# Optimization experiments

Measured on AMD Instinct MI355X. Metric: run time of the kernel, lower is better.

## Reference

```python
import jax, jax.numpy as jnp
import numpy as np

B = 16384          # batch
IN = 256           # input_dim
HID = [1024, 1024, 512]
K = 8              # num_mixtures
D = 16             # latent_dim
NT = D * (D + 1) // 2  # 136 packed tril components per mixture

_rows, _cols = np.tril_indices(D)          # row-major lower-tri order, same as nested loops
_rows = jnp.asarray(_rows); _cols = jnp.asarray(_cols)
_diag_mask = _rows == _cols                # [NT] bool


def setup_inputs() -> dict:
    key = jax.random.key(0)
    ks = jax.random.split(key, 12)

    def lin(k, fi, fo):
        kw, kb = jax.random.split(k)
        s = 1.0 / np.sqrt(fi)
        W = (jax.random.uniform(kw, (fi, fo), minval=-s, maxval=s)).astype(jnp.float32)
        b = (jax.random.uniform(kb, (fo,), minval=-s, maxval=s)).astype(jnp.float32)
        return W, b

    W0, b0 = lin(ks[0], IN, HID[0])
    W1, b1 = lin(ks[1], HID[0], HID[1])
    W2, b2 = lin(ks[2], HID[1], HID[2])
    Wpi, bpi = lin(ks[3], HID[2], K)
    Wmu, bmu = lin(ks[4], HID[2], K * D)
    Wt, bt = lin(ks[5], HID[2], K * NT)
    x = jax.random.normal(ks[6], (B, IN), dtype=jnp.float32)
    return dict(x=x, W0=W0, b0=b0, W1=W1, b1=b1, W2=W2, b2=b2,
                Wpi=Wpi, bpi=bpi, Wmu=Wmu, bmu=bmu, Wt=Wt, bt=bt)


def reference(x, W0, b0, W1, b1, W2, b2, Wpi, bpi, Wmu, bmu, Wt, bt):
    # MLP trunk: Linear + ReLU chain
    h = jax.nn.relu(x @ W0 + b0)
    h = jax.nn.relu(h @ W1 + b1)
    h = jax.nn.relu(h @ W2 + b2)
    # Heads
    pi_k = jax.nn.softmax(h @ Wpi + bpi, axis=1)                 # [B, K]
    mu_k = (h @ Wmu + bmu).reshape(-1, K, D)                     # [B, K, D]
    tc = (h @ Wt + bt).reshape(-1, K, NT)                        # [B, K, NT]
    # Fused cholesky-tril assembly: exp on diagonal entries, copy off-diagonal,
    # scattered into lower triangle in row-major (i, j<=i) order.
    vals = jnp.where(_diag_mask, jnp.exp(tc), tc)                # [B, K, NT]
    tril = jnp.zeros((tc.shape[0], K, D, D), dtype=tc.dtype)
    tril = tril.at[:, :, _rows, _cols].set(vals)                 # [B, K, D, D]
    return pi_k, mu_k, tril
```

## Files before the change

### kernel.cpp

```cpp
#include <hip/hip_runtime.h>
#include <hip/hip_bf16.h>
#include <cstdint>
#include <cstddef>

typedef __attribute__((ext_vector_type(8))) _Float16 half8;
typedef __attribute__((ext_vector_type(4))) float f32x4;
typedef __attribute__((ext_vector_type(8))) unsigned short ushort8v;
typedef __attribute__((ext_vector_type(4))) unsigned short ushort4v;

__device__ __forceinline__ unsigned short f2h_bits(float x) {
  _Float16 h = (_Float16)x;
  union { _Float16 h; unsigned short u; } cv; cv.h = h; return cv.u;
}

__device__ __forceinline__ void barrier_raw() {
  asm volatile("" ::: "memory");
  __builtin_amdgcn_s_barrier();
  asm volatile("" ::: "memory");
}
template<int N> __device__ __forceinline__ void vmw() {
  static_assert(N == 0 || N == 3 || N == 4, "unsupported vmcnt");
  if constexpr (N == 0) asm volatile("s_waitcnt vmcnt(0)" ::: "memory");
  if constexpr (N == 3) asm volatile("s_waitcnt vmcnt(3)" ::: "memory");
  if constexpr (N == 4) asm volatile("s_waitcnt vmcnt(4)" ::: "memory");
}
__device__ __forceinline__ void lgkm0() {
  asm volatile("s_waitcnt lgkmcnt(0)" ::: "memory");
}


__global__ __launch_bounds__(256) void k_f32_to_f16(const float* __restrict__ src,
                                                    unsigned short* __restrict__ dst, int n4) {
  int i = blockIdx.x * 256 + threadIdx.x;
  if (i >= n4) return;
  float4 v = ((const float4*)src)[i];
  ushort4v o;
  o[0] = f2h_bits(v.x); o[1] = f2h_bits(v.y); o[2] = f2h_bits(v.z); o[3] = f2h_bits(v.w);
  ((ushort4v*)dst)[i] = o;
}

__global__ __launch_bounds__(256) void k_transpose_f16(const float* __restrict__ W,
                                                       unsigned short* __restrict__ Wt,
                                                       int Kd, int N) {
  int tid = blockIdx.x * 256 + threadIdx.x;
  int total = (Kd >> 3) * N;
  if (tid >= total) return;
  int kc = tid / N;
  int n  = tid - kc * N;
  int k0 = kc << 3;
  ushort8v o;
#pragma unroll
  for (int j = 0; j < 8; ++j) o[j] = f2h_bits(W[(size_t)(k0 + j) * N + n]);
  *(ushort8v*)(&Wt[(size_t)n * Kd + k0]) = o;
}

__global__ __launch_bounds__(256) void k_build_head(
    const float* __restrict__ Wmu, const float* __restrict__ Wt,
    const float* __restrict__ Wpi,
    const float* __restrict__ bmu, const float* __restrict__ bt,
    const float* __restrict__ bpi,
    unsigned short* __restrict__ whd, float* __restrict__ bhd)
{
  int tid = blockIdx.x * 256 + threadIdx.x;
  if (tid >= 2304 * 64) return;
  int r  = tid >> 6;
  int d0 = (tid & 63) << 3;

  const float* src = nullptr; int stride = 0;
  if (r < 128) { src = Wmu + r; stride = 128; }
  else if (r < 2176) {
    int rU = r - 128, k = rU >> 8, i = (rU >> 4) & 15, j = rU & 15;
    if (j <= i) { src = Wt + k * 136 + ((i * (i + 1)) >> 1) + j; stride = 1088; }
  } else if (r < 2184) { src = Wpi + (r - 2176); stride = 8; }

  ushort8v o;
#pragma unroll
  for (int jj = 0; jj < 8; ++jj)
    o[jj] = src ? f2h_bits(src[(size_t)(d0 + jj) * stride]) : (unsigned short)0;
  *(ushort8v*)(&whd[(size_t)r * 512 + d0]) = o;

  if (d0 == 0) {
    float b = 0.f;
    if (r < 128) b = bmu[r];
    else if (r < 2176) {
      int rU = r - 128, k = rU >> 8, i = (rU >> 4) & 15, j = rU & 15;
      if (j <= i) b = bt[k * 136 + ((i * (i + 1)) >> 1) + j];
    } else if (r < 2184) b = bpi[r - 2176];
    bhd[r] = b;
  }
}


__device__ __forceinline__ void epi_relu_h(const f32x4& a, const float* bias, int col0,
                                           unsigned short* Hout, size_t row, int N) {
  float4 b4 = *(const float4*)&bias[col0];
  ushort4v o;
  float v0 = a[0] + b4.x; o[0] = f2h_bits(v0 > 0.f ? v0 : 0.f);
  float v1 = a[1] + b4.y; o[1] = f2h_bits(v1 > 0.f ? v1 : 0.f);
  float v2 = a[2] + b4.z; o[2] = f2h_bits(v2 > 0.f ? v2 : 0.f);
  float v3 = a[3] + b4.w; o[3] = f2h_bits(v3 > 0.f ? v3 : 0.f);
  *(ushort4v*)&Hout[row * N + col0] = o;
}

__device__ __forceinline__ void epi_head(const f32x4& a, const float* bias, int col0,
                                         size_t row, float* out_pi, float* out_mu,
                                         float* out_tril) {
  if (col0 >= 2184) return;
  float4 b4 = *(const float4*)&bias[col0];
  float v[4] = { a[0] + b4.x, a[1] + b4.y, a[2] + b4.z, a[3] + b4.w };
  if (col0 < 128) {
    *(float4*)&out_mu[row * 128 + col0] = make_float4(v[0], v[1], v[2], v[3]);
  } else if (col0 < 2176) {
    const int cc0 = col0 - 128;
    const int i   = (cc0 >> 4) & 15;
    const int j0  = cc0 & 15;
#pragma unroll
    for (int r = 0; r < 4; ++r) if (j0 + r == i) v[r] = expf(v[r]);
    *(float4*)&out_tril[row * 2048 + cc0] = make_float4(v[0], v[1], v[2], v[3]);
  } else {
    float m4 = fmaxf(fmaxf(v[0], v[1]), fmaxf(v[2], v[3]));
    float mx = fmaxf(m4, __shfl_xor(m4, 16));
    float e[4], s4 = 0.f;
#pragma unroll
    for (int r = 0; r < 4; ++r) { e[r] = expf(v[r] - mx); s4 += e[r]; }
    float sm = s4 + __shfl_xor(s4, 16);
    *(float4*)&out_pi[row * 8 + (col0 - 2176)] =
        make_float4(e[0] / sm, e[1] / sm, e[2] / sm, e[3] / sm);
  }
}


template<int EPI>
__global__ __launch_bounds__(256) void k_gemm3b(
    const unsigned short* __restrict__ A,
    const unsigned short* __restrict__ Bt,
    int Kd, int N, int nNb,
    const float* __restrict__ bias,
    unsigned short* __restrict__ Hout,
    float* __restrict__ out_pi,
    float* __restrict__ out_mu,
    float* __restrict__ out_tril)
{
  __shared__ unsigned short Ald[3][128 * 32];
  __shared__ unsigned short Bld[3][128 * 32];

  const int tid  = threadIdx.x;
  const int lane = tid & 63;
  const int wv   = tid >> 6;
  const int wr   = wv >> 1;
  const int wc   = wv & 1;
  const int l15  = lane & 15;
  const int lk   = lane >> 4;

  const int cpx = gridDim.x >> 3;
  const int bid = blockIdx.x;
  const int swz = (bid & 7) * cpx + (bid >> 3);
  const int bm  = (swz / nNb) << 7;
  const int bn  = (swz % nNb) << 7;

  f32x4 acc[4][4] = {};

  const unsigned short* aBase = A  + (size_t)bm * Kd;
  const unsigned short* bBase = Bt + (size_t)bn * Kd;

  const int xo = ((lk ^ ((l15 >> 1) & 3)) << 3);

  auto stage = [&](int bb, int kt) {
    const int k0 = kt << 5;
#pragma unroll
    for (int i = 0; i < 2; ++i) {
      const int cbase = (wv << 6) + (i << 8);
      const int c_    = cbase + lane;
      const int row   = c_ >> 2;
      const int sc    = (((c_ & 3) ^ ((c_ >> 3) & 3)) << 3);
      __builtin_amdgcn_global_load_lds(
          (const __attribute__((address_space(1))) void*)(aBase + (size_t)row * Kd + k0 + sc),
          (__attribute__((address_space(3))) void*)(&Ald[bb][cbase << 3]),
          16, 0, 0);
      __builtin_amdgcn_global_load_lds(
          (const __attribute__((address_space(1))) void*)(bBase + (size_t)row * Kd + k0 + sc),
          (__attribute__((address_space(3))) void*)(&Bld[bb][cbase << 3]),
          16, 0, 0);
    }
  };

  const int nk = Kd >> 5;
  stage(0, 0);
  stage(1, 1);
  vmw<4>();
  barrier_raw();

  int i0 = 0, i1 = 1, i2 = 2;
  for (int kt = 0; kt < nk; ++kt) {
    if (kt + 2 < nk) stage(i2, kt + 2);

    half8 af[4], bfr[4];
#pragma unroll
    for (int m = 0; m < 4; ++m)
      af[m]  = *(const half8*)&Ald[i0][((wr << 6) + (m << 4) + l15) * 32 + xo];
#pragma unroll
    for (int n = 0; n < 4; ++n)
      bfr[n] = *(const half8*)&Bld[i0][((wc << 6) + (n << 4) + l15) * 32 + xo];

    __builtin_amdgcn_s_setprio(1);
#pragma unroll
    for (int m = 0; m < 4; ++m)
#pragma unroll
      for (int n = 0; n < 4; ++n)
        acc[m][n] = __builtin_amdgcn_mfma_f32_16x16x32_f16(bfr[n], af[m], acc[m][n], 0, 0, 0);
    __builtin_amdgcn_s_setprio(0);

    if (kt + 1 < nk) {
      if (kt + 2 < nk) vmw<4>();
      else             vmw<0>();
      barrier_raw();
    }
    const int t = i0; i0 = i1; i1 = i2; i2 = t;
  }

#pragma unroll
  for (int m = 0; m < 4; ++m) {
    const size_t row = bm + (wr << 6) + (m << 4) + l15;
#pragma unroll
    for (int n = 0; n < 4; ++n) {
      const int col0 = bn + (wc << 6) + (n << 4) + (lk << 2);
      if (EPI == 0) epi_relu_h(acc[m][n], bias, col0, Hout, row, N);
      else          epi_head(acc[m][n], bias, col0, row, out_pi, out_mu, out_tril);
    }
  }
}


template<int NH, int M_rep>
__device__ __forceinline__ void mfma_phase(const half8* af, const half8* bf,
                                           f32x4 (*acc)[4]) {
  __builtin_amdgcn_s_setprio(1);
#pragma unroll
  for (int m = 0; m < M_rep; ++m) {
    acc[m][NH * 2 + 0] = __builtin_amdgcn_mfma_f32_16x16x32_f16(bf[0], af[m], acc[m][NH * 2 + 0], 0, 0, 0);
    acc[m][NH * 2 + 1] = __builtin_amdgcn_mfma_f32_16x16x32_f16(bf[1], af[m], acc[m][NH * 2 + 1], 0, 0, 0);
  }
  __builtin_amdgcn_s_setprio(0);
}

template<int BM, int BN>
__global__ __launch_bounds__(512) void k_gemm8p(
    const unsigned short* __restrict__ A,
    const unsigned short* __restrict__ Bt,
    int Kd, int N, int nNb,
    const float* __restrict__ bias,
    unsigned short* __restrict__ Hout)
{
  constexpr int M_rep = BM / 32;
  constexpr int A_LD  = BM / 128;
  constexpr int B_LD  = BN / 128;
  constexpr int WN    = A_LD + B_LD;

  __shared__ unsigned short Ald[2][2][BM * 32];
  __shared__ unsigned short Bld[2][2][BN * 32];

  const int tid  = threadIdx.x;
  const int lane = tid & 63;
  const int wid  = tid >> 6;
  const int wm   = wid >> 2;
  const int wn   = wid & 3;
  const int l15  = lane & 15;
  const int lk   = lane >> 4;

  const int cpx = gridDim.x >> 3;
  const int bid = blockIdx.x;
  const int swz = (bid & 7) * cpx + (bid >> 3);
  const int bm  = (swz / nNb) * BM;
  const int bn  = (swz % nNb) * BN;

  const unsigned short* aBase = A  + (size_t)bm * Kd;
  const unsigned short* bBase = Bt + (size_t)bn * Kd;

  f32x4 acc[M_rep][4] = {};

  const int xo   = ((lk ^ ((l15 >> 1) & 3)) << 3);
  const int rowA = wm * (BM / 2) + l15;
  const int colB = wn * 64 + l15;

  auto stageA = [&](int bb, int h, int k0) {
#pragma unroll
    for (int i = 0; i < A_LD; ++i) {
      const int cbase = (wid << 6) + (i << 9);
      const int c_    = cbase + lane;
      const int row   = c_ >> 2;
      const int sc    = (((c_ & 3) ^ ((c_ >> 3) & 3)) << 3);
      __builtin_amdgcn_global_load_lds(
          (const __attribute__((address_space(1))) void*)(aBase + (size_t)row * Kd + k0 + h * 32 + sc),
          (__attribute__((address_space(3))) void*)(&Ald[bb][h][(size_t)cbase << 3]),
          16, 0, 0);
    }
  };
  auto stageB = [&](int bb, int h, int k0) {
#pragma unroll
    for (int i = 0; i < B_LD; ++i) {
      const int cbase = (wid << 6) + (i << 9);
      const int c_    = cbase + lane;
      const int row   = c_ >> 2;
      const int sc    = (((c_ & 3) ^ ((c_ >> 3) & 3)) << 3);
      __builtin_amdgcn_global_load_lds(
          (const __attribute__((address_space(1))) void*)(bBase + (size_t)row * Kd + k0 + h * 32 + sc),
          (__attribute__((address_space(3))) void*)(&Bld[bb][h][(size_t)cbase << 3]),
          16, 0, 0);
    }
  };

#define RD_A(kk)                                                                 \
  {                                                                              \
    _Pragma("unroll")                                                            \
    for (int m = 0; m < M_rep; ++m)                                              \
      af[m] = *(const half8*)&Ald[cur][kk][(size_t)(rowA + m * 16) * 32 + xo];   \
  }
#define RD_B(kk, nh)                                                             \
  {                                                                              \
    _Pragma("unroll")                                                            \
    for (int n2 = 0; n2 < 2; ++n2)                                               \
      bf[n2] = *(const half8*)&Bld[cur][kk][(size_t)(colB + ((nh) * 2 + n2) * 16) * 32 + xo]; \
  }

  const int nk = Kd >> 6;
  stageA(0, 0, 0); stageB(0, 0, 0); stageA(0, 1, 0); stageB(0, 1, 0);
  vmw<WN>();
  barrier_raw();

  int cur = 0;
  for (int kt = 0; kt < nk; ++kt) {
    const bool pre = (kt + 1 < nk);
    const int  k0n = (kt + 1) << 6;
    half8 af[M_rep], bf[2];

    RD_A(0); RD_B(0, 0);
    if (pre) stageA(cur ^ 1, 0, k0n);
    barrier_raw(); lgkm0();
    mfma_phase<0, M_rep>(af, bf, acc);
    barrier_raw();

    RD_B(0, 1);
    if (pre) stageB(cur ^ 1, 0, k0n);
    barrier_raw(); lgkm0();
    mfma_phase<1, M_rep>(af, bf, acc);
    if (pre) vmw<WN>(); else vmw<0>();
    barrier_raw();

    RD_A(1); RD_B(1, 0);
    if (pre) stageA(cur ^ 1, 1, k0n);
    barrier_raw(); lgkm0();
    mfma_phase<0, M_rep>(af, bf, acc);
    barrier_raw();

    RD_B(1, 1);
    if (pre) stageB(cur ^ 1, 1, k0n);
    barrier_raw(); lgkm0();
    mfma_phase<1, M_rep>(af, bf, acc);
    if (pre) vmw<WN>();
    barrier_raw();

    cur ^= 1;
  }
#undef RD_A
#undef RD_B

#pragma unroll
  for (int m = 0; m < M_rep; ++m) {
    const size_t row = bm + wm * (BM / 2) + (m << 4) + l15;
#pragma unroll
    for (int n = 0; n < 4; ++n) {
      const int col0 = bn + wn * 64 + (n << 4) + (lk << 2);
      epi_relu_h(acc[m][n], bias, col0, Hout, row, N);
    }
  }
}


extern "C" void kernel_launch(void* const* d_in, const int* in_sizes, int n_in,
                              void* d_out, int out_size, void* d_ws, size_t ws_size,
                              hipStream_t stream)
{
  const float* x   = (const float*)d_in[0];
  const float* W0  = (const float*)d_in[1];
  const float* b0  = (const float*)d_in[2];
  const float* W1  = (const float*)d_in[3];
  const float* b1  = (const float*)d_in[4];
  const float* W2  = (const float*)d_in[5];
  const float* b2  = (const float*)d_in[6];
  const float* Wpi = (const float*)d_in[7];
  const float* bpi = (const float*)d_in[8];
  const float* Wmu = (const float*)d_in[9];
  const float* bmu = (const float*)d_in[10];
  const float* Wt  = (const float*)d_in[11];
  const float* bt  = (const float*)d_in[12];

  char* ws = (char*)d_ws;
  unsigned short* xh  = (unsigned short*)(ws);
  unsigned short* h0  = (unsigned short*)(ws + 8388608);
  unsigned short* h1  = (unsigned short*)(ws + 41943040);
  unsigned short* h2  = (unsigned short*)(ws + 8388608);
  unsigned short* w0b = (unsigned short*)(ws + 75497472);
  unsigned short* w1b = (unsigned short*)(ws + 76021760);
  unsigned short* w2b = (unsigned short*)(ws + 78118912);
  unsigned short* whd = (unsigned short*)(ws + 79167488);
  float*          bhd = (float*)         (ws + 81526784);

  float* out_pi   = (float*)d_out;
  float* out_mu   = (float*)d_out + 131072;
  float* out_tril = (float*)d_out + 2228224;

  k_f32_to_f16<<<4096, 256, 0, stream>>>(x, xh, 1048576);
  k_transpose_f16<<<128, 256, 0, stream>>>(W0, w0b, 256, 1024);
  k_transpose_f16<<<512, 256, 0, stream>>>(W1, w1b, 1024, 1024);
  k_transpose_f16<<<256, 256, 0, stream>>>(W2, w2b, 1024, 512);
  k_build_head<<<576, 256, 0, stream>>>(Wmu, Wt, Wpi, bmu, bt, bpi, whd, bhd);

  k_gemm3b<0><<<1024, 256, 0, stream>>>(xh, w0b, 256, 1024, 8, b0, h0,
                                        nullptr, nullptr, nullptr);
  k_gemm8p<256, 256><<<256, 512, 0, stream>>>(h0, w1b, 1024, 1024, 4, b1, h1);
  k_gemm8p<128, 256><<<256, 512, 0, stream>>>(h1, w2b, 1024, 512, 2, b2, h2);
  k_gemm3b<1><<<2304, 256, 0, stream>>>(h2, whd, 512, 2304, 18, bhd, nullptr,
                                        out_pi, out_mu, out_tril);
}
```

Before: 185.9 us.

## Replace LDS-tiled head GEMM with register-direct MFMA kernel on pre-swizzled weights

Head weights are now pre-packed into the exact per-lane MFMA fragment order, and head columns are padded to 2240 instead of 2304. A new head kernel loads A and B fragments straight from global memory into registers with double buffering, skipping LDS staging and barriers. Blocks are swizzled across 35 column strips so neighbouring blocks share A rows in cache. The aim is to cut LDS traffic, synchronisation and padded work in the output-bound head GEMM. The cost is heavier global and L2 load traffic with no LDS reuse across waves.

```diff
diff --git a/kernel.cpp b/kernel.cpp
--- a/kernel.cpp
+++ b/kernel.cpp
@@ -59,12 +59,13 @@
     const float* __restrict__ Wpi,
     const float* __restrict__ bmu, const float* __restrict__ bt,
     const float* __restrict__ bpi,
-    unsigned short* __restrict__ whd, float* __restrict__ bhd)
+    unsigned short* __restrict__ bsh, float* __restrict__ bhd)
 {
   int tid = blockIdx.x * 256 + threadIdx.x;
-  if (tid >= 2304 * 64) return;
+  if (tid >= 2240 * 64) return;
   int r  = tid >> 6;
-  int d0 = (tid & 63) << 3;
+  int o  = tid & 63;
+  int d0 = o << 3;
 
   const float* src = nullptr; int stride = 0;
   if (r < 128) { src = Wmu + r; stride = 128; }
@@ -73,13 +74,21 @@
     if (j <= i) { src = Wt + k * 136 + ((i * (i + 1)) >> 1) + j; stride = 1088; }
   } else if (r < 2184) { src = Wpi + (r - 2176); stride = 8; }
 
-  ushort8v o;
+  ushort8v ov;
 #pragma unroll
   for (int jj = 0; jj < 8; ++jj)
-    o[jj] = src ? f2h_bits(src[(size_t)(d0 + jj) * stride]) : (unsigned short)0;
-  *(ushort8v*)(&whd[(size_t)r * 512 + d0]) = o;
-
-  if (d0 == 0) {
+    ov[jj] = src ? f2h_bits(src[(size_t)(d0 + jj) * stride]) : (unsigned short)0;
+
+  const int strip = r >> 6;
+  const int n     = (r >> 4) & 3;
+  const int l15   = r & 15;
+  const int t     = o >> 2;
+  const int lk    = o & 3;
+  const int lane  = (lk << 4) | l15;
+  const size_t off = ((((size_t)(strip * 16 + t) * 4 + n) * 64) + lane) * 8;
+  *(ushort8v*)(&bsh[off]) = ov;
+
+  if (o == 0) {
     float b = 0.f;
     if (r < 128) b = bmu[r];
     else if (r < 2176) {
@@ -126,6 +135,77 @@
     float sm = s4 + __shfl_xor(s4, 16);
     *(float4*)&out_pi[row * 8 + (col0 - 2176)] =
         make_float4(e[0] / sm, e[1] / sm, e[2] / sm, e[3] / sm);
+  }
+}
+
+
+template<int NK>
+__global__ __launch_bounds__(256, 3) void k_flat_head(
+    const unsigned short* __restrict__ A,
+    const unsigned short* __restrict__ Bs,
+    const float* __restrict__ bias,
+    float* __restrict__ out_pi,
+    float* __restrict__ out_mu,
+    float* __restrict__ out_tril)
+{
+  const int tid  = threadIdx.x;
+  const int lane = tid & 63;
+  const int wv   = tid >> 6;
+  const int l15  = lane & 15;
+  const int lk   = lane >> 4;
+
+  constexpr int nStrip = 35;
+  const int cpx = gridDim.x >> 3;
+  const int bid = blockIdx.x;
+  const int swz = (bid & 7) * cpx + (bid >> 3);
+  const int bmi   = swz / nStrip;
+  const int strip = swz % nStrip;
+  const int row0  = bmi * 256 + wv * 64;
+
+  const unsigned short* aP = A  + (size_t)(row0 + l15) * 512 + lk * 8;
+  const unsigned short* bP = Bs + ((size_t)strip * NK * 4 * 64 + (size_t)lane) * 8;
+
+  f32x4 acc[4][4] = {};
+
+  half8 aE[4], bE[4], aO[4], bO[4];
+
+  auto LDA = [&](half8* a, int t) {
+#pragma unroll
+    for (int m = 0; m < 4; ++m)
+      a[m] = *(const half8*)(aP + (size_t)m * 16 * 512 + t * 32);
+  };
+  auto LDB = [&](half8* b, int t) {
+#pragma unroll
+    for (int n = 0; n < 4; ++n)
+      b[n] = *(const half8*)(bP + (size_t)t * 2048 + n * 512);
+  };
+  auto STEP = [&](const half8* a, const half8* b) {
+    __builtin_amdgcn_s_setprio(1);
+#pragma unroll
+    for (int m = 0; m < 4; ++m)
+#pragma unroll
+      for (int n = 0; n < 4; ++n)
+        acc[m][n] = __builtin_amdgcn_mfma_f32_16x16x32_f16(b[n], a[m], acc[m][n], 0, 0, 0);
+    __builtin_amdgcn_s_setprio(0);
+  };
+
+  LDA(aE, 0); LDB(bE, 0);
+#pragma unroll
+  for (int tp = 0; tp < NK / 2; ++tp) {
+    LDA(aO, 2 * tp + 1); LDB(bO, 2 * tp + 1);
+    STEP(aE, bE);
+    if (2 * tp + 2 < NK) { LDA(aE, 2 * tp + 2); LDB(bE, 2 * tp + 2); }
+    STEP(aO, bO);
+  }
+
+#pragma unroll
+  for (int m = 0; m < 4; ++m) {
+    const size_t row = row0 + (m << 4) + l15;
+#pragma unroll
+    for (int n = 0; n < 4; ++n) {
+      const int col0 = strip * 64 + (n << 4) + (lk << 2);
+      epi_head(acc[m][n], bias, col0, row, out_pi, out_mu, out_tril);
+    }
   }
 }
 
@@ -402,7 +482,7 @@
   unsigned short* w0b = (unsigned short*)(ws + 75497472);
   unsigned short* w1b = (unsigned short*)(ws + 76021760);
   unsigned short* w2b = (unsigned short*)(ws + 78118912);
-  unsigned short* whd = (unsigned short*)(ws + 79167488);
+  unsigned short* bsh = (unsigned short*)(ws + 79167488);
   float*          bhd = (float*)         (ws + 81526784);
 
   float* out_pi   = (float*)d_out;
@@ -413,12 +493,11 @@
   k_transpose_f16<<<128, 256, 0, stream>>>(W0, w0b, 256, 1024);
   k_transpose_f16<<<512, 256, 0, stream>>>(W1, w1b, 1024, 1024);
   k_transpose_f16<<<256, 256, 0, stream>>>(W2, w2b, 1024, 512);
-  k_build_head<<<576, 256, 0, stream>>>(Wmu, Wt, Wpi, bmu, bt, bpi, whd, bhd);
+  k_build_head<<<560, 256, 0, stream>>>(Wmu, Wt, Wpi, bmu, bt, bpi, bsh, bhd);
 
   k_gemm3b<0><<<1024, 256, 0, stream>>>(xh, w0b, 256, 1024, 8, b0, h0,
                                         nullptr, nullptr, nullptr);
   k_gemm8p<256, 256><<<256, 512, 0, stream>>>(h0, w1b, 1024, 1024, 4, b1, h1);
   k_gemm8p<128, 256><<<256, 512, 0, stream>>>(h1, w2b, 1024, 512, 2, b2, h2);
-  k_gemm3b<1><<<2304, 256, 0, stream>>>(h2, whd, 512, 2304, 18, bhd, nullptr,
-                                        out_pi, out_mu, out_tril);
-}
+  k_flat_head<16><<<2240, 256, 0, stream>>>(h2, bsh, bhd, out_pi, out_mu, out_tril);
+}
```

Result: slower. 222.0 us (+19.4%).

## Compact head GEMM columns to skip all-zero upper-triangle 4-wide tiles

Applied to the files above, without the earlier changes.

The head weight matrix is rebuilt so each mixture uses 160 columns covering only the 4-wide column groups that touch the lower triangle, instead of the full 256-column 16x16 layout. This shrinks the head GEMM N dimension from 2304 to 1536, and the epilogue maps each compacted column back to its (i, j) position in the output. A separate kernel writes zeros into the upper-triangle float4 groups that are no longer produced. The cost is an extra launch and some index arithmetic in the epilogue.

```diff
diff --git a/kernel.cpp b/kernel.cpp
--- a/kernel.cpp
+++ b/kernel.cpp
@@ -54,6 +54,13 @@
   *(ushort8v*)(&Wt[(size_t)n * Kd + k0]) = o;
 }
 
+__device__ __forceinline__ void q_to_ij(int q, int& i, int& j) {
+  if (q < 16)      { i = q >> 2;              j = q & 3; }
+  else if (q < 48) { i = 4 + ((q - 16) >> 3); j = (q - 16) & 7; }
+  else if (q < 96) { int u = q - 48; int d = u / 12; i = 8 + d;  j = u - 12 * d; }
+  else             { i = 12 + ((q - 96) >> 4); j = (q - 96) & 15; }
+}
+
 __global__ __launch_bounds__(256) void k_build_head(
     const float* __restrict__ Wmu, const float* __restrict__ Wt,
     const float* __restrict__ Wpi,
@@ -62,16 +69,17 @@
     unsigned short* __restrict__ whd, float* __restrict__ bhd)
 {
   int tid = blockIdx.x * 256 + threadIdx.x;
-  if (tid >= 2304 * 64) return;
+  if (tid >= 1536 * 64) return;
   int r  = tid >> 6;
   int d0 = (tid & 63) << 3;
 
   const float* src = nullptr; int stride = 0;
   if (r < 128) { src = Wmu + r; stride = 128; }
-  else if (r < 2176) {
-    int rU = r - 128, k = rU >> 8, i = (rU >> 4) & 15, j = rU & 15;
+  else if (r < 1408) {
+    int rr = r - 128, k = rr / 160, q = rr - k * 160, i, j;
+    q_to_ij(q, i, j);
     if (j <= i) { src = Wt + k * 136 + ((i * (i + 1)) >> 1) + j; stride = 1088; }
-  } else if (r < 2184) { src = Wpi + (r - 2176); stride = 8; }
+  } else if (r < 1416) { src = Wpi + (r - 1408); stride = 8; }
 
   ushort8v o;
 #pragma unroll
@@ -82,12 +90,28 @@
   if (d0 == 0) {
     float b = 0.f;
     if (r < 128) b = bmu[r];
-    else if (r < 2176) {
-      int rU = r - 128, k = rU >> 8, i = (rU >> 4) & 15, j = rU & 15;
+    else if (r < 1408) {
+      int rr = r - 128, k = rr / 160, q = rr - k * 160, i, j;
+      q_to_ij(q, i, j);
       if (j <= i) b = bt[k * 136 + ((i * (i + 1)) >> 1) + j];
-    } else if (r < 2184) b = bpi[r - 2176];
+    } else if (r < 1416) b = bpi[r - 1408];
     bhd[r] = b;
   }
+}
+
+__global__ __launch_bounds__(256) void k_zero_tail(float* __restrict__ out_tril, int total) {
+  int tid = blockIdx.x * 256 + threadIdx.x;
+  if (tid >= total) return;
+  int row = tid / 192;
+  int rem = tid - row * 192;
+  int k   = rem / 24;
+  int z   = rem - k * 24;
+  int i, j0;
+  if (z < 12)      { i = z / 3;            j0 = 4 + 4 * (z - 3 * i); }
+  else if (z < 20) { int u = z - 12; i = 4 + (u >> 1); j0 = 8 + 4 * (u & 1); }
+  else             { i = 8 + (z - 20);     j0 = 12; }
+  *(float4*)&out_tril[(size_t)row * 2048 + (k << 8) + (i << 4) + j0] =
+      make_float4(0.f, 0.f, 0.f, 0.f);
 }
 
 
@@ -105,18 +129,21 @@
 __device__ __forceinline__ void epi_head(const f32x4& a, const float* bias, int col0,
                                          size_t row, float* out_pi, float* out_mu,
                                          float* out_tril) {
-  if (col0 >= 2184) return;
+  if (col0 >= 1416) return;
   float4 b4 = *(const float4*)&bias[col0];
   float v[4] = { a[0] + b4.x, a[1] + b4.y, a[2] + b4.z, a[3] + b4.w };
   if (col0 < 128) {
     *(float4*)&out_mu[row * 128 + col0] = make_float4(v[0], v[1], v[2], v[3]);
-  } else if (col0 < 2176) {
-    const int cc0 = col0 - 128;
-    const int i   = (cc0 >> 4) & 15;
-    const int j0  = cc0 & 15;
+  } else if (col0 < 1408) {
+    const int cc = col0 - 128;
+    const int k  = cc / 160;
+    const int q  = cc - k * 160;
+    int i, j0;
+    q_to_ij(q, i, j0);
 #pragma unroll
     for (int r = 0; r < 4; ++r) if (j0 + r == i) v[r] = expf(v[r]);
-    *(float4*)&out_tril[row * 2048 + cc0] = make_float4(v[0], v[1], v[2], v[3]);
+    *(float4*)&out_tril[row * 2048 + (k << 8) + (i << 4) + j0] =
+        make_float4(v[0], v[1], v[2], v[3]);
   } else {
     float m4 = fmaxf(fmaxf(v[0], v[1]), fmaxf(v[2], v[3]));
     float mx = fmaxf(m4, __shfl_xor(m4, 16));
@@ -124,7 +151,7 @@
 #pragma unroll
     for (int r = 0; r < 4; ++r) { e[r] = expf(v[r] - mx); s4 += e[r]; }
     float sm = s4 + __shfl_xor(s4, 16);
-    *(float4*)&out_pi[row * 8 + (col0 - 2176)] =
+    *(float4*)&out_pi[row * 8 + (col0 - 1408)] =
         make_float4(e[0] / sm, e[1] / sm, e[2] / sm, e[3] / sm);
   }
 }
@@ -413,12 +440,13 @@
   k_transpose_f16<<<128, 256, 0, stream>>>(W0, w0b, 256, 1024);
   k_transpose_f16<<<512, 256, 0, stream>>>(W1, w1b, 1024, 1024);
   k_transpose_f16<<<256, 256, 0, stream>>>(W2, w2b, 1024, 512);
-  k_build_head<<<576, 256, 0, stream>>>(Wmu, Wt, Wpi, bmu, bt, bpi, whd, bhd);
+  k_build_head<<<384, 256, 0, stream>>>(Wmu, Wt, Wpi, bmu, bt, bpi, whd, bhd);
 
   k_gemm3b<0><<<1024, 256, 0, stream>>>(xh, w0b, 256, 1024, 8, b0, h0,
                                         nullptr, nullptr, nullptr);
   k_gemm8p<256, 256><<<256, 512, 0, stream>>>(h0, w1b, 1024, 1024, 4, b1, h1);
   k_gemm8p<128, 256><<<256, 512, 0, stream>>>(h1, w2b, 1024, 512, 2, b2, h2);
-  k_gemm3b<1><<<2304, 256, 0, stream>>>(h2, whd, 512, 2304, 18, bhd, nullptr,
+  k_zero_tail<<<12288, 256, 0, stream>>>(out_tril, 16384 * 8 * 24);
+  k_gemm3b<1><<<1536, 256, 0, stream>>>(h2, whd, 512, 1536, 12, bhd, nullptr,
                                         out_pi, out_mu, out_tril);
 }
```

Measured after the change: 191.5 us. +3.0%, slower.
